# Optimization experiments

Hardware: AMD Instinct MI355X
Metric: run time of the kernel (lower is better)

## Reference

```python
import jax, jax.numpy as jnp
import numpy as np

GAMMA = 0.1
B, C, H, W = 8, 64, 64, 64
CINT = C // 8


def setup_inputs() -> dict:
    key = jax.random.key(0)
    ks = jax.random.split(key, 5)
    x = jax.random.normal(ks[0], (B, C, H, W), dtype=jnp.float32)
    Wq = jax.random.normal(ks[1], (CINT, C), dtype=jnp.float32) * 0.05
    Wk = jax.random.normal(ks[2], (CINT, C), dtype=jnp.float32) * 0.05
    Wv = jax.random.normal(ks[3], (CINT, C), dtype=jnp.float32) * 0.05
    Wout = jax.random.normal(ks[4], (C, CINT), dtype=jnp.float32) * 0.05
    return {"x": x, "Wq": Wq, "Wk": Wk, "Wv": Wv, "Wout": Wout}


def reference(x, Wq, Wk, Wv, Wout):
    b, c, h, w = x.shape
    n = h * w
    cint = Wq.shape[0]
    xf = x.reshape(b, c, n)                               # [B,C,N]
    q = jnp.einsum('ic,bcn->bin', Wq, xf)                 # [B,Cint,N]
    k = jnp.einsum('ic,bcn->bin', Wk, xf)
    v = jnp.einsum('ic,bcn->bin', Wv, xf)
    # scores[b, n, m] = q[b,:,n] . k[b,:,m]; softmax over dim=1 (the n axis)
    scores = jnp.einsum('bin,bim->bnm', q, k) / jnp.sqrt(jnp.asarray(cint, x.dtype))
    att = jax.nn.softmax(scores, axis=1)                  # [B,N,N], softmax over rows
    att_out = jnp.einsum('bin,bnm->bim', v, att)          # [B,Cint,N]
    out = jnp.einsum('ci,bim->bcm', Wout, att_out)        # [B,C,N]
    return x + out.reshape(b, c, h, w) * GAMMA
```

## Files before the change

### kernel.cpp

```cpp
#include <hip/hip_runtime.h>
#include <math.h>

#define BB 8
#define CC 64
#define NN 4096
#define CI 8
#define GAMMA 0.1f
#define SCALE (1.44269504088896f * 0.35355339059327f)
#define NSPLIT 4

typedef float v4f __attribute__((ext_vector_type(4)));
typedef __bf16 bf16x8 __attribute__((ext_vector_type(8)));
typedef __bf16 bf16x4 __attribute__((ext_vector_type(4)));
typedef __bf16 bf16x2 __attribute__((ext_vector_type(2)));

__device__ __forceinline__ float fast_exp2(float x) {
    return __builtin_amdgcn_exp2f(x);
}

__global__ __launch_bounds__(256) void qkv_kernel(
        const float* __restrict__ x,
        const float* __restrict__ Wq, const float* __restrict__ Wk,
        const float* __restrict__ Wv,
        __bf16* __restrict__ qbh, __bf16* __restrict__ kbh,
        __bf16* __restrict__ vbh, float* __restrict__ attab) {
    __shared__ float sw[3 * CI * CC];
    __shared__ unsigned short sq[32 * 8];
    __shared__ unsigned short sk[32 * 8];
    const int t = threadIdx.x;
    const int i  = t >> 5;
    const int nl = t & 31;
    const int b  = blockIdx.y;
    const int n0 = blockIdx.x * 32;

    for (int idx = t; idx < CI * CC; idx += 256) {
        sw[idx]                = Wq[idx];
        sw[CI * CC + idx]      = Wk[idx] * SCALE;
        sw[2 * CI * CC + idx]  = Wv[idx];
    }
    int lin = (blockIdx.y * (NN / 32) + blockIdx.x) * 256 + t;
    for (int idx = lin; idx < BB * 9 * NN; idx += BB * NN * CI) attab[idx] = 0.f;
    __syncthreads();

    const int n = n0 + nl;
    const float* xp = x + ((size_t)b * CC) * NN + n;
    const v4f* wq4 = (const v4f*)(sw + i * CC);
    const v4f* wk4 = (const v4f*)(sw + CI * CC + i * CC);
    const v4f* wv4 = (const v4f*)(sw + 2 * CI * CC + i * CC);
    float qa = 0.f, ka = 0.f, va = 0.f;
#pragma unroll 4
    for (int c4 = 0; c4 < CC / 4; ++c4) {
        v4f wq = wq4[c4], wk = wk4[c4], wv = wv4[c4];
        float x0 = xp[(size_t)(c4 * 4 + 0) * NN];
        float x1 = xp[(size_t)(c4 * 4 + 1) * NN];
        float x2 = xp[(size_t)(c4 * 4 + 2) * NN];
        float x3 = xp[(size_t)(c4 * 4 + 3) * NN];
        qa = fmaf(wq.x, x0, qa); ka = fmaf(wk.x, x0, ka); va = fmaf(wv.x, x0, va);
        qa = fmaf(wq.y, x1, qa); ka = fmaf(wk.y, x1, ka); va = fmaf(wv.y, x1, va);
        qa = fmaf(wq.z, x2, qa); ka = fmaf(wk.z, x2, ka); va = fmaf(wv.z, x2, va);
        qa = fmaf(wq.w, x3, qa); ka = fmaf(wk.w, x3, ka); va = fmaf(wv.w, x3, va);
    }
    __bf16 vb = (__bf16)va;
    vbh[((size_t)b * CI + i) * NN + n] = vb;
    __bf16 qb = (__bf16)qa, kb2 = (__bf16)ka;
    sq[nl * 8 + i] = *(unsigned short*)&qb;
    sk[nl * 8 + i] = *(unsigned short*)&kb2;
    __syncthreads();
    if (t < 32) {
        *(uint4*)(qbh + ((size_t)b * NN + n0 + t) * 8) = *(const uint4*)(sq + t * 8);
        *(uint4*)(kbh + ((size_t)b * NN + n0 + t) * 8) = *(const uint4*)(sk + t * 8);
    }
}

__global__ __launch_bounds__(256) void att_kernel(
        const __bf16* __restrict__ qbh, const __bf16* __restrict__ kbh,
        const __bf16* __restrict__ vbh, float* __restrict__ attab) {
    __shared__ unsigned short eld[4][16 * 36];
    const int t = threadIdx.x;
    const int w    = t >> 6;
    const int l    = t & 63;
    const int quad = l >> 4;
    const int lm   = l & 15;
    const int b  = blockIdx.z;
    const int m0 = blockIdx.x * 64 + w * 16;
    const int nbase = blockIdx.y * (NN / NSPLIT);

    bf16x8 zero8, ones8;
#pragma unroll
    for (int z = 0; z < 8; ++z) { zero8[z] = (__bf16)0.0f; ones8[z] = (__bf16)1.0f; }

    bf16x8 kfrag = zero8;
    if (quad == 0)
        kfrag = *(const bf16x8*)(kbh + ((size_t)b * NN + m0 + lm) * 8);

    const __bf16* vrow = vbh + ((size_t)b * CI + (lm & 7)) * NN;

    v4f accO = {0.f, 0.f, 0.f, 0.f};
    unsigned short* ew = &eld[w][lm * 36];

    for (int ch = 0; ch < (NN / NSPLIT) / 32; ++ch) {
        const int nc = nbase + ch * 32;
        bf16x8 q0 = zero8, q1 = zero8;
        if (quad == 0) {
            q0 = *(const bf16x8*)(qbh + ((size_t)b * NN + nc + lm) * 8);
            q1 = *(const bf16x8*)(qbh + ((size_t)b * NN + nc + 16 + lm) * 8);
        }
        bf16x8 vfrag;
        if (lm < 8)      vfrag = *(const bf16x8*)(vrow + nc + quad * 8);
        else if (lm == 8) vfrag = ones8;
        else              vfrag = zero8;

        v4f s0 = __builtin_amdgcn_mfma_f32_16x16x32_bf16(q0, kfrag, (v4f){0.f,0.f,0.f,0.f}, 0, 0, 0);
        v4f s1 = __builtin_amdgcn_mfma_f32_16x16x32_bf16(q1, kfrag, (v4f){0.f,0.f,0.f,0.f}, 0, 0, 0);

        bf16x2 p;
        p[0] = (__bf16)fast_exp2(s0.x); p[1] = (__bf16)fast_exp2(s0.y);
        *(bf16x2*)(ew + quad * 4 + 0)  = p;
        p[0] = (__bf16)fast_exp2(s0.z); p[1] = (__bf16)fast_exp2(s0.w);
        *(bf16x2*)(ew + quad * 4 + 2)  = p;
        p[0] = (__bf16)fast_exp2(s1.x); p[1] = (__bf16)fast_exp2(s1.y);
        *(bf16x2*)(ew + 16 + quad * 4 + 0) = p;
        p[0] = (__bf16)fast_exp2(s1.z); p[1] = (__bf16)fast_exp2(s1.w);
        *(bf16x2*)(ew + 16 + quad * 4 + 2) = p;

        const unsigned short* er = ew + quad * 8;
        bf16x4 e_lo = *(const bf16x4*)(er);
        bf16x4 e_hi = *(const bf16x4*)(er + 4);
        bf16x8 efrag;
#pragma unroll
        for (int z = 0; z < 4; ++z) { efrag[z] = e_lo[z]; efrag[4 + z] = e_hi[z]; }

        accO = __builtin_amdgcn_mfma_f32_16x16x32_bf16(vfrag, efrag, accO, 0, 0, 0);
    }

    float* ap = attab + (size_t)b * 9 * NN + m0 + lm;
    float av[4] = {accO.x, accO.y, accO.z, accO.w};
#pragma unroll
    for (int r = 0; r < 4; ++r) {
        int i = quad * 4 + r;
        if (i < 9) atomicAdd(ap + (size_t)i * NN, av[r]);
    }
}

__global__ __launch_bounds__(256) void out_kernel(
        const float* __restrict__ x, const float* __restrict__ Wout,
        const float* __restrict__ attab, float* __restrict__ out) {
    const int t = threadIdx.x;
    const int c = blockIdx.y;
    const int b = blockIdx.z;
    const int m = (blockIdx.x * 256 + t) * 4;
    const float* ap = attab + (size_t)b * 9 * NN + m;
    v4f sum = *(const v4f*)(ap + (size_t)8 * NN);
    v4f s = {0.f, 0.f, 0.f, 0.f};
#pragma unroll
    for (int i = 0; i < CI; ++i) {
        float wgt = Wout[c * CI + i];
        v4f a = *(const v4f*)(ap + (size_t)i * NN);
        s.x = fmaf(wgt, a.x, s.x);
        s.y = fmaf(wgt, a.y, s.y);
        s.z = fmaf(wgt, a.z, s.z);
        s.w = fmaf(wgt, a.w, s.w);
    }
    size_t o = ((size_t)b * CC + c) * NN + m;
    v4f xv = *(const v4f*)(x + o);
    v4f r;
    r.x = xv.x + GAMMA * (s.x / sum.x);
    r.y = xv.y + GAMMA * (s.y / sum.y);
    r.z = xv.z + GAMMA * (s.z / sum.z);
    r.w = xv.w + GAMMA * (s.w / sum.w);
    *(v4f*)(out + o) = r;
}

extern "C" void kernel_launch(void* const* d_in, const int* in_sizes, int n_in,
                              void* d_out, int out_size, void* d_ws, size_t ws_size,
                              hipStream_t stream) {
    const float* x    = (const float*)d_in[0];
    const float* Wq   = (const float*)d_in[1];
    const float* Wk   = (const float*)d_in[2];
    const float* Wv   = (const float*)d_in[3];
    const float* Wout = (const float*)d_in[4];
    float* out = (float*)d_out;

    __bf16* qbh = (__bf16*)d_ws;
    __bf16* kbh = qbh + (size_t)BB * NN * 8;
    __bf16* vbh = kbh + (size_t)BB * NN * 8;
    float* attab = (float*)(vbh + (size_t)BB * NN * 8);

    qkv_kernel<<<dim3(NN / 32, BB), 256, 0, stream>>>(x, Wq, Wk, Wv, qbh, kbh, vbh, attab);
    att_kernel<<<dim3(NN / 64, NSPLIT, BB), 256, 0, stream>>>(qbh, kbh, vbh, attab);
    out_kernel<<<dim3(NN / 1024, CC, BB), 256, 0, stream>>>(x, Wout, attab, out);
}
```

Baseline: 114.4 us.

## Fuse three kernels into one persistent cooperative kernel with grid syncs

Merges the QKV projection, attention and output kernels into a single cooperative persistent kernel that uses grid.sync between phases, looping over tiles with a grid sized from occupancy. It also restructures the attention inner loop to process two chunks at a time through double-buffered LDS with wider stores. This removes the launch gaps between kernels, but adds grid-wide barrier cost, a per-call occupancy query on the host, and may lower occupancy because all phases share one register and LDS budget.

```diff
diff --git a/kernel.cpp b/kernel.cpp
--- a/kernel.cpp
+++ b/kernel.cpp
@@ -1,5 +1,8 @@
 #include <hip/hip_runtime.h>
+#include <hip/hip_cooperative_groups.h>
 #include <math.h>
+
+namespace cg = cooperative_groups;
 
 #define BB 8
 #define CC 64
@@ -12,163 +15,168 @@
 typedef float v4f __attribute__((ext_vector_type(4)));
 typedef __bf16 bf16x8 __attribute__((ext_vector_type(8)));
 typedef __bf16 bf16x4 __attribute__((ext_vector_type(4)));
-typedef __bf16 bf16x2 __attribute__((ext_vector_type(2)));
 
 __device__ __forceinline__ float fast_exp2(float x) {
     return __builtin_amdgcn_exp2f(x);
 }
 
-__global__ __launch_bounds__(256) void qkv_kernel(
+__global__ __launch_bounds__(256) void fused_kernel(
         const float* __restrict__ x,
         const float* __restrict__ Wq, const float* __restrict__ Wk,
-        const float* __restrict__ Wv,
+        const float* __restrict__ Wv, const float* __restrict__ Wout,
         __bf16* __restrict__ qbh, __bf16* __restrict__ kbh,
-        __bf16* __restrict__ vbh, float* __restrict__ attab) {
-    __shared__ float sw[3 * CI * CC];
-    __shared__ unsigned short sq[32 * 8];
-    __shared__ unsigned short sk[32 * 8];
+        __bf16* __restrict__ vbh, float* __restrict__ attab,
+        float* __restrict__ out) {
+    __shared__ __align__(16) char smem[10240];
+    cg::grid_group grid = cg::this_grid();
     const int t = threadIdx.x;
-    const int i  = t >> 5;
-    const int nl = t & 31;
-    const int b  = blockIdx.y;
-    const int n0 = blockIdx.x * 32;
-
-    for (int idx = t; idx < CI * CC; idx += 256) {
-        sw[idx]                = Wq[idx];
-        sw[CI * CC + idx]      = Wk[idx] * SCALE;
-        sw[2 * CI * CC + idx]  = Wv[idx];
+    const int nblk = gridDim.x;
+
+    {
+        float* sw = (float*)smem;
+        unsigned short* sq = (unsigned short*)(smem + 6144);
+        unsigned short* sk = sq + 256;
+        for (int idx = blockIdx.x * 256 + t; idx < BB * 9 * NN; idx += nblk * 256)
+            attab[idx] = 0.f;
+        for (int idx = t; idx < CI * CC; idx += 256) {
+            sw[idx]        = Wq[idx];
+            sw[512 + idx]  = Wk[idx] * SCALE;
+            sw[1024 + idx] = Wv[idx];
+        }
+        __syncthreads();
+        const int i  = t >> 5;
+        const int nl = t & 31;
+        for (int tile = blockIdx.x; tile < BB * (NN / 32); tile += nblk) {
+            const int b  = tile >> 7;
+            const int n0 = (tile & 127) * 32;
+            const int n  = n0 + nl;
+            const float* xp = x + ((size_t)b * CC) * NN + n;
+            const v4f* wq4 = (const v4f*)(sw + i * CC);
+            const v4f* wk4 = (const v4f*)(sw + 512 + i * CC);
+            const v4f* wv4 = (const v4f*)(sw + 1024 + i * CC);
+            float qa = 0.f, ka = 0.f, va = 0.f;
+#pragma unroll 4
+            for (int c4 = 0; c4 < CC / 4; ++c4) {
+                v4f wq = wq4[c4], wk = wk4[c4], wv = wv4[c4];
+                float x0 = xp[(size_t)(c4 * 4 + 0) * NN];
+                float x1 = xp[(size_t)(c4 * 4 + 1) * NN];
+                float x2 = xp[(size_t)(c4 * 4 + 2) * NN];
+                float x3 = xp[(size_t)(c4 * 4 + 3) * NN];
+                qa = fmaf(wq.x, x0, qa); ka = fmaf(wk.x, x0, ka); va = fmaf(wv.x, x0, va);
+                qa = fmaf(wq.y, x1, qa); ka = fmaf(wk.y, x1, ka); va = fmaf(wv.y, x1, va);
+                qa = fmaf(wq.z, x2, qa); ka = fmaf(wk.z, x2, ka); va = fmaf(wv.z, x2, va);
+                qa = fmaf(wq.w, x3, qa); ka = fmaf(wk.w, x3, ka); va = fmaf(wv.w, x3, va);
+            }
+            __bf16 vb = (__bf16)va;
+            vbh[((size_t)b * CI + i) * NN + n] = vb;
+            __bf16 qb = (__bf16)qa, kb2 = (__bf16)ka;
+            sq[nl * 8 + i] = *(unsigned short*)&qb;
+            sk[nl * 8 + i] = *(unsigned short*)&kb2;
+            __syncthreads();
+            if (t < 32) {
+                *(uint4*)(qbh + ((size_t)b * NN + n0 + t) * 8) = *(const uint4*)(sq + t * 8);
+                *(uint4*)(kbh + ((size_t)b * NN + n0 + t) * 8) = *(const uint4*)(sk + t * 8);
+            }
+            __syncthreads();
+        }
     }
-    int lin = (blockIdx.y * (NN / 32) + blockIdx.x) * 256 + t;
-    for (int idx = lin; idx < BB * 9 * NN; idx += BB * NN * CI) attab[idx] = 0.f;
-    __syncthreads();
-
-    const int n = n0 + nl;
-    const float* xp = x + ((size_t)b * CC) * NN + n;
-    const v4f* wq4 = (const v4f*)(sw + i * CC);
-    const v4f* wk4 = (const v4f*)(sw + CI * CC + i * CC);
-    const v4f* wv4 = (const v4f*)(sw + 2 * CI * CC + i * CC);
-    float qa = 0.f, ka = 0.f, va = 0.f;
-#pragma unroll 4
-    for (int c4 = 0; c4 < CC / 4; ++c4) {
-        v4f wq = wq4[c4], wk = wk4[c4], wv = wv4[c4];
-        float x0 = xp[(size_t)(c4 * 4 + 0) * NN];
-        float x1 = xp[(size_t)(c4 * 4 + 1) * NN];
-        float x2 = xp[(size_t)(c4 * 4 + 2) * NN];
-        float x3 = xp[(size_t)(c4 * 4 + 3) * NN];
-        qa = fmaf(wq.x, x0, qa); ka = fmaf(wk.x, x0, ka); va = fmaf(wv.x, x0, va);
-        qa = fmaf(wq.y, x1, qa); ka = fmaf(wk.y, x1, ka); va = fmaf(wv.y, x1, va);
-        qa = fmaf(wq.z, x2, qa); ka = fmaf(wk.z, x2, ka); va = fmaf(wv.z, x2, va);
-        qa = fmaf(wq.w, x3, qa); ka = fmaf(wk.w, x3, ka); va = fmaf(wv.w, x3, va);
+    grid.sync();
+
+    {
+        const int w    = t >> 6;
+        const int l    = t & 63;
+        const int quad = l >> 4;
+        const int lm   = l & 15;
+        unsigned short* buf0 = (unsigned short*)smem + w * 1280;
+        unsigned short* buf1 = buf0 + 640;
+
+        bf16x8 zero8, ones8;
+#pragma unroll
+        for (int z = 0; z < 8; ++z) { zero8[z] = (__bf16)0.0f; ones8[z] = (__bf16)1.0f; }
+
+        for (int u = blockIdx.x; u < BB * NSPLIT * (NN / 64); u += nblk) {
+            const int b     = u >> 8;
+            const int nbase = ((u >> 6) & (NSPLIT - 1)) * (NN / NSPLIT);
+            const int m0    = (u & 63) * 64 + w * 16;
+
+            bf16x8 kfrag = zero8;
+            if (quad == 0)
+                kfrag = *(const bf16x8*)(kbh + ((size_t)b * NN + m0 + lm) * 8);
+            const __bf16* vrow = vbh + ((size_t)b * CI + (lm & 7)) * NN;
+            const __bf16* qrow = qbh + (size_t)b * NN * 8;
+
+            v4f accO = {0.f, 0.f, 0.f, 0.f};
+
+            auto stage1 = [&](int nc, unsigned short* buf, bf16x8& vfrag) {
+                bf16x8 q0 = zero8, q1 = zero8;
+                if (quad == 0) {
+                    q0 = *(const bf16x8*)(qrow + (size_t)(nc + lm) * 8);
+                    q1 = *(const bf16x8*)(qrow + (size_t)(nc + 16 + lm) * 8);
+                }
+                if (lm < 8)       vfrag = *(const bf16x8*)(vrow + nc + quad * 8);
+                else if (lm == 8) vfrag = ones8;
+                else              vfrag = zero8;
+                v4f s0 = __builtin_amdgcn_mfma_f32_16x16x32_bf16(q0, kfrag, (v4f){0.f,0.f,0.f,0.f}, 0, 0, 0);
+                v4f s1 = __builtin_amdgcn_mfma_f32_16x16x32_bf16(q1, kfrag, (v4f){0.f,0.f,0.f,0.f}, 0, 0, 0);
+                bf16x4 e0, e1;
+                e0[0] = (__bf16)fast_exp2(s0.x); e0[1] = (__bf16)fast_exp2(s0.y);
+                e0[2] = (__bf16)fast_exp2(s0.z); e0[3] = (__bf16)fast_exp2(s0.w);
+                e1[0] = (__bf16)fast_exp2(s1.x); e1[1] = (__bf16)fast_exp2(s1.y);
+                e1[2] = (__bf16)fast_exp2(s1.z); e1[3] = (__bf16)fast_exp2(s1.w);
+                *(bf16x4*)(buf + lm * 40 + quad * 4)      = e0;
+                *(bf16x4*)(buf + lm * 40 + 16 + quad * 4) = e1;
+            };
+            auto stage2 = [&](unsigned short* buf, bf16x8 vfrag) {
+                bf16x8 efrag = *(const bf16x8*)(buf + lm * 40 + quad * 8);
+                accO = __builtin_amdgcn_mfma_f32_16x16x32_bf16(vfrag, efrag, accO, 0, 0, 0);
+            };
+
+            for (int ch = 0; ch < (NN / NSPLIT) / 32; ch += 2) {
+                bf16x8 vf0, vf1;
+                stage1(nbase + ch * 32, buf0, vf0);
+                stage1(nbase + (ch + 1) * 32, buf1, vf1);
+                stage2(buf0, vf0);
+                stage2(buf1, vf1);
+            }
+
+            float* ap = attab + (size_t)b * 9 * NN + m0 + lm;
+            float av[4] = {accO.x, accO.y, accO.z, accO.w};
+#pragma unroll
+            for (int r = 0; r < 4; ++r) {
+                int i = quad * 4 + r;
+                if (i < 9) atomicAdd(ap + (size_t)i * NN, av[r]);
+            }
+        }
     }
-    __bf16 vb = (__bf16)va;
-    vbh[((size_t)b * CI + i) * NN + n] = vb;
-    __bf16 qb = (__bf16)qa, kb2 = (__bf16)ka;
-    sq[nl * 8 + i] = *(unsigned short*)&qb;
-    sk[nl * 8 + i] = *(unsigned short*)&kb2;
-    __syncthreads();
-    if (t < 32) {
-        *(uint4*)(qbh + ((size_t)b * NN + n0 + t) * 8) = *(const uint4*)(sq + t * 8);
-        *(uint4*)(kbh + ((size_t)b * NN + n0 + t) * 8) = *(const uint4*)(sk + t * 8);
+    grid.sync();
+
+    for (int q = blockIdx.x * 256 + t; q < BB * CC * (NN / 4); q += nblk * 256) {
+        const int m4   = q & (NN / 4 - 1);
+        const int rest = q >> 10;
+        const int c = rest & (CC - 1);
+        const int b = rest >> 6;
+        const int m = m4 * 4;
+        const float* ap = attab + (size_t)b * 9 * NN + m;
+        v4f sum = *(const v4f*)(ap + (size_t)8 * NN);
+        v4f s = {0.f, 0.f, 0.f, 0.f};
+#pragma unroll
+        for (int i = 0; i < CI; ++i) {
+            float wgt = Wout[c * CI + i];
+            v4f a = *(const v4f*)(ap + (size_t)i * NN);
+            s.x = fmaf(wgt, a.x, s.x);
+            s.y = fmaf(wgt, a.y, s.y);
+            s.z = fmaf(wgt, a.z, s.z);
+            s.w = fmaf(wgt, a.w, s.w);
+        }
+        size_t o = ((size_t)b * CC + c) * NN + m;
+        v4f xv = *(const v4f*)(x + o);
+        v4f r;
+        r.x = xv.x + GAMMA * (s.x / sum.x);
+        r.y = xv.y + GAMMA * (s.y / sum.y);
+        r.z = xv.z + GAMMA * (s.z / sum.z);
+        r.w = xv.w + GAMMA * (s.w / sum.w);
+        *(v4f*)(out + o) = r;
     }
-}
-
-__global__ __launch_bounds__(256) void att_kernel(
-        const __bf16* __restrict__ qbh, const __bf16* __restrict__ kbh,
-        const __bf16* __restrict__ vbh, float* __restrict__ attab) {
-    __shared__ unsigned short eld[4][16 * 36];
-    const int t = threadIdx.x;
-    const int w    = t >> 6;
-    const int l    = t & 63;
-    const int quad = l >> 4;
-    const int lm   = l & 15;
-    const int b  = blockIdx.z;
-    const int m0 = blockIdx.x * 64 + w * 16;
-    const int nbase = blockIdx.y * (NN / NSPLIT);
-
-    bf16x8 zero8, ones8;
-#pragma unroll
-    for (int z = 0; z < 8; ++z) { zero8[z] = (__bf16)0.0f; ones8[z] = (__bf16)1.0f; }
-
-    bf16x8 kfrag = zero8;
-    if (quad == 0)
-        kfrag = *(const bf16x8*)(kbh + ((size_t)b * NN + m0 + lm) * 8);
-
-    const __bf16* vrow = vbh + ((size_t)b * CI + (lm & 7)) * NN;
-
-    v4f accO = {0.f, 0.f, 0.f, 0.f};
-    unsigned short* ew = &eld[w][lm * 36];
-
-    for (int ch = 0; ch < (NN / NSPLIT) / 32; ++ch) {
-        const int nc = nbase + ch * 32;
-        bf16x8 q0 = zero8, q1 = zero8;
-        if (quad == 0) {
-            q0 = *(const bf16x8*)(qbh + ((size_t)b * NN + nc + lm) * 8);
-            q1 = *(const bf16x8*)(qbh + ((size_t)b * NN + nc + 16 + lm) * 8);
-        }
-        bf16x8 vfrag;
-        if (lm < 8)      vfrag = *(const bf16x8*)(vrow + nc + quad * 8);
-        else if (lm == 8) vfrag = ones8;
-        else              vfrag = zero8;
-
-        v4f s0 = __builtin_amdgcn_mfma_f32_16x16x32_bf16(q0, kfrag, (v4f){0.f,0.f,0.f,0.f}, 0, 0, 0);
-        v4f s1 = __builtin_amdgcn_mfma_f32_16x16x32_bf16(q1, kfrag, (v4f){0.f,0.f,0.f,0.f}, 0, 0, 0);
-
-        bf16x2 p;
-        p[0] = (__bf16)fast_exp2(s0.x); p[1] = (__bf16)fast_exp2(s0.y);
-        *(bf16x2*)(ew + quad * 4 + 0)  = p;
-        p[0] = (__bf16)fast_exp2(s0.z); p[1] = (__bf16)fast_exp2(s0.w);
-        *(bf16x2*)(ew + quad * 4 + 2)  = p;
-        p[0] = (__bf16)fast_exp2(s1.x); p[1] = (__bf16)fast_exp2(s1.y);
-        *(bf16x2*)(ew + 16 + quad * 4 + 0) = p;
-        p[0] = (__bf16)fast_exp2(s1.z); p[1] = (__bf16)fast_exp2(s1.w);
-        *(bf16x2*)(ew + 16 + quad * 4 + 2) = p;
-
-        const unsigned short* er = ew + quad * 8;
-        bf16x4 e_lo = *(const bf16x4*)(er);
-        bf16x4 e_hi = *(const bf16x4*)(er + 4);
-        bf16x8 efrag;
-#pragma unroll
-        for (int z = 0; z < 4; ++z) { efrag[z] = e_lo[z]; efrag[4 + z] = e_hi[z]; }
-
-        accO = __builtin_amdgcn_mfma_f32_16x16x32_bf16(vfrag, efrag, accO, 0, 0, 0);
-    }
-
-    float* ap = attab + (size_t)b * 9 * NN + m0 + lm;
-    float av[4] = {accO.x, accO.y, accO.z, accO.w};
-#pragma unroll
-    for (int r = 0; r < 4; ++r) {
-        int i = quad * 4 + r;
-        if (i < 9) atomicAdd(ap + (size_t)i * NN, av[r]);
-    }
-}
-
-__global__ __launch_bounds__(256) void out_kernel(
-        const float* __restrict__ x, const float* __restrict__ Wout,
-        const float* __restrict__ attab, float* __restrict__ out) {
-    const int t = threadIdx.x;
-    const int c = blockIdx.y;
-    const int b = blockIdx.z;
-    const int m = (blockIdx.x * 256 + t) * 4;
-    const float* ap = attab + (size_t)b * 9 * NN + m;
-    v4f sum = *(const v4f*)(ap + (size_t)8 * NN);
-    v4f s = {0.f, 0.f, 0.f, 0.f};
-#pragma unroll
-    for (int i = 0; i < CI; ++i) {
-        float wgt = Wout[c * CI + i];
-        v4f a = *(const v4f*)(ap + (size_t)i * NN);
-        s.x = fmaf(wgt, a.x, s.x);
-        s.y = fmaf(wgt, a.y, s.y);
-        s.z = fmaf(wgt, a.z, s.z);
-        s.w = fmaf(wgt, a.w, s.w);
-    }
-    size_t o = ((size_t)b * CC + c) * NN + m;
-    v4f xv = *(const v4f*)(x + o);
-    v4f r;
-    r.x = xv.x + GAMMA * (s.x / sum.x);
-    r.y = xv.y + GAMMA * (s.y / sum.y);
-    r.z = xv.z + GAMMA * (s.z / sum.z);
-    r.w = xv.w + GAMMA * (s.w / sum.w);
-    *(v4f*)(out + o) = r;
 }
 
 extern "C" void kernel_launch(void* const* d_in, const int* in_sizes, int n_in,
@@ -186,7 +194,14 @@
     __bf16* vbh = kbh + (size_t)BB * NN * 8;
     float* attab = (float*)(vbh + (size_t)BB * NN * 8);
 
-    qkv_kernel<<<dim3(NN / 32, BB), 256, 0, stream>>>(x, Wq, Wk, Wv, qbh, kbh, vbh, attab);
-    att_kernel<<<dim3(NN / 64, NSPLIT, BB), 256, 0, stream>>>(qbh, kbh, vbh, attab);
-    out_kernel<<<dim3(NN / 1024, CC, BB), 256, 0, stream>>>(x, Wout, attab, out);
+    int occ = 0;
+    hipOccupancyMaxActiveBlocksPerMultiprocessor(&occ, fused_kernel, 256, 0);
+    if (occ < 1) occ = 1;
+    int gridn = occ * 256;
+    if (gridn > 2048) gridn = 2048;
+
+    void* args[] = {(void*)&x, (void*)&Wq, (void*)&Wk, (void*)&Wv, (void*)&Wout,
+                    (void*)&qbh, (void*)&kbh, (void*)&vbh, (void*)&attab, (void*)&out};
+    hipLaunchCooperativeKernel((const void*)fused_kernel, dim3(gridn), dim3(256),
+                               args, 0, stream);
 }
```

Measured after the change: 239.3 us. 2.09x slower.

## Replace second MFMA with per-lane packed FMA accumulation of exp-weighted V

Applied to the files above, without the earlier changes.

Drops the LDS round trip and the second MFMA that multiplied V by the exp-scores. Each lane now exponentiates its own score elements and accumulates them against fp32 V rows with packed v2 FMAs, then reduces across quads with shuffles before the atomics. V is stored as fp32 in an [n][8] layout so each lane can load contiguous vectors. The V@P product moves from matrix cores to vector ALU work, and V reads per lane grow because fp32 V is loaded for every score element.

```diff
diff --git a/kernel.cpp b/kernel.cpp
--- a/kernel.cpp
+++ b/kernel.cpp
@@ -9,10 +9,9 @@
 #define SCALE (1.44269504088896f * 0.35355339059327f)
 #define NSPLIT 4
 
+typedef float v2f __attribute__((ext_vector_type(2)));
 typedef float v4f __attribute__((ext_vector_type(4)));
 typedef __bf16 bf16x8 __attribute__((ext_vector_type(8)));
-typedef __bf16 bf16x4 __attribute__((ext_vector_type(4)));
-typedef __bf16 bf16x2 __attribute__((ext_vector_type(2)));
 
 __device__ __forceinline__ float fast_exp2(float x) {
     return __builtin_amdgcn_exp2f(x);
@@ -23,10 +22,11 @@
         const float* __restrict__ Wq, const float* __restrict__ Wk,
         const float* __restrict__ Wv,
         __bf16* __restrict__ qbh, __bf16* __restrict__ kbh,
-        __bf16* __restrict__ vbh, float* __restrict__ attab) {
+        float* __restrict__ vf, float* __restrict__ attab) {
     __shared__ float sw[3 * CI * CC];
     __shared__ unsigned short sq[32 * 8];
     __shared__ unsigned short sk[32 * 8];
+    __shared__ float sv[32 * 8];
     const int t = threadIdx.x;
     const int i  = t >> 5;
     const int nl = t & 31;
@@ -60,22 +60,25 @@
         qa = fmaf(wq.z, x2, qa); ka = fmaf(wk.z, x2, ka); va = fmaf(wv.z, x2, va);
         qa = fmaf(wq.w, x3, qa); ka = fmaf(wk.w, x3, ka); va = fmaf(wv.w, x3, va);
     }
-    __bf16 vb = (__bf16)va;
-    vbh[((size_t)b * CI + i) * NN + n] = vb;
     __bf16 qb = (__bf16)qa, kb2 = (__bf16)ka;
     sq[nl * 8 + i] = *(unsigned short*)&qb;
     sk[nl * 8 + i] = *(unsigned short*)&kb2;
+    sv[nl * 8 + i] = va;
     __syncthreads();
     if (t < 32) {
         *(uint4*)(qbh + ((size_t)b * NN + n0 + t) * 8) = *(const uint4*)(sq + t * 8);
         *(uint4*)(kbh + ((size_t)b * NN + n0 + t) * 8) = *(const uint4*)(sk + t * 8);
     }
+    if (t < 64) {
+        int n2 = t >> 1, h = t & 1;
+        *(v4f*)(vf + ((size_t)b * NN + n0 + n2) * 8 + h * 4) =
+            *(const v4f*)(sv + n2 * 8 + h * 4);
+    }
 }
 
 __global__ __launch_bounds__(256) void att_kernel(
         const __bf16* __restrict__ qbh, const __bf16* __restrict__ kbh,
-        const __bf16* __restrict__ vbh, float* __restrict__ attab) {
-    __shared__ unsigned short eld[4][16 * 36];
+        const float* __restrict__ vf, float* __restrict__ attab) {
     const int t = threadIdx.x;
     const int w    = t >> 6;
     const int l    = t & 63;
@@ -85,60 +88,72 @@
     const int m0 = blockIdx.x * 64 + w * 16;
     const int nbase = blockIdx.y * (NN / NSPLIT);
 
-    bf16x8 zero8, ones8;
-#pragma unroll
-    for (int z = 0; z < 8; ++z) { zero8[z] = (__bf16)0.0f; ones8[z] = (__bf16)1.0f; }
+    bf16x8 zero8;
+#pragma unroll
+    for (int z = 0; z < 8; ++z) zero8[z] = (__bf16)0.0f;
 
     bf16x8 kfrag = zero8;
     if (quad == 0)
         kfrag = *(const bf16x8*)(kbh + ((size_t)b * NN + m0 + lm) * 8);
 
-    const __bf16* vrow = vbh + ((size_t)b * CI + (lm & 7)) * NN;
-
-    v4f accO = {0.f, 0.f, 0.f, 0.f};
-    unsigned short* ew = &eld[w][lm * 36];
-
+    const __bf16* qrow = qbh + (size_t)b * NN * 8;
+    const float*  vrow = vf  + (size_t)b * NN * 8;
+
+    v2f acc[4] = {(v2f){0.f,0.f}, (v2f){0.f,0.f}, (v2f){0.f,0.f}, (v2f){0.f,0.f}};
+    float es = 0.f;
+
+#pragma unroll 2
     for (int ch = 0; ch < (NN / NSPLIT) / 32; ++ch) {
         const int nc = nbase + ch * 32;
         bf16x8 q0 = zero8, q1 = zero8;
         if (quad == 0) {
-            q0 = *(const bf16x8*)(qbh + ((size_t)b * NN + nc + lm) * 8);
-            q1 = *(const bf16x8*)(qbh + ((size_t)b * NN + nc + 16 + lm) * 8);
+            q0 = *(const bf16x8*)(qrow + (size_t)(nc + lm) * 8);
+            q1 = *(const bf16x8*)(qrow + (size_t)(nc + 16 + lm) * 8);
         }
-        bf16x8 vfrag;
-        if (lm < 8)      vfrag = *(const bf16x8*)(vrow + nc + quad * 8);
-        else if (lm == 8) vfrag = ones8;
-        else              vfrag = zero8;
-
         v4f s0 = __builtin_amdgcn_mfma_f32_16x16x32_bf16(q0, kfrag, (v4f){0.f,0.f,0.f,0.f}, 0, 0, 0);
         v4f s1 = __builtin_amdgcn_mfma_f32_16x16x32_bf16(q1, kfrag, (v4f){0.f,0.f,0.f,0.f}, 0, 0, 0);
 
-        bf16x2 p;
-        p[0] = (__bf16)fast_exp2(s0.x); p[1] = (__bf16)fast_exp2(s0.y);
-        *(bf16x2*)(ew + quad * 4 + 0)  = p;
-        p[0] = (__bf16)fast_exp2(s0.z); p[1] = (__bf16)fast_exp2(s0.w);
-        *(bf16x2*)(ew + quad * 4 + 2)  = p;
-        p[0] = (__bf16)fast_exp2(s1.x); p[1] = (__bf16)fast_exp2(s1.y);
-        *(bf16x2*)(ew + 16 + quad * 4 + 0) = p;
-        p[0] = (__bf16)fast_exp2(s1.z); p[1] = (__bf16)fast_exp2(s1.w);
-        *(bf16x2*)(ew + 16 + quad * 4 + 2) = p;
-
-        const unsigned short* er = ew + quad * 8;
-        bf16x4 e_lo = *(const bf16x4*)(er);
-        bf16x4 e_hi = *(const bf16x4*)(er + 4);
-        bf16x8 efrag;
-#pragma unroll
-        for (int z = 0; z < 4; ++z) { efrag[z] = e_lo[z]; efrag[4 + z] = e_hi[z]; }
-
-        accO = __builtin_amdgcn_mfma_f32_16x16x32_bf16(vfrag, efrag, accO, 0, 0, 0);
-    }
-
-    float* ap = attab + (size_t)b * 9 * NN + m0 + lm;
-    float av[4] = {accO.x, accO.y, accO.z, accO.w};
-#pragma unroll
-    for (int r = 0; r < 4; ++r) {
-        int i = quad * 4 + r;
-        if (i < 9) atomicAdd(ap + (size_t)i * NN, av[r]);
+        const float* vp0 = vrow + (size_t)(nc + quad * 4) * 8;
+        const float* vp1 = vrow + (size_t)(nc + 16 + quad * 4) * 8;
+        float sv0[4] = {s0.x, s0.y, s0.z, s0.w};
+        float sv1[4] = {s1.x, s1.y, s1.z, s1.w};
+#pragma unroll
+        for (int r = 0; r < 4; ++r) {
+            float e = fast_exp2(sv0[r]);
+            es += e;
+            v4f vlo = *(const v4f*)(vp0 + r * 8);
+            v4f vhi = *(const v4f*)(vp0 + r * 8 + 4);
+            v2f e2 = {e, e};
+            acc[0] = __builtin_elementwise_fma(e2, (v2f){vlo.x, vlo.y}, acc[0]);
+            acc[1] = __builtin_elementwise_fma(e2, (v2f){vlo.z, vlo.w}, acc[1]);
+            acc[2] = __builtin_elementwise_fma(e2, (v2f){vhi.x, vhi.y}, acc[2]);
+            acc[3] = __builtin_elementwise_fma(e2, (v2f){vhi.z, vhi.w}, acc[3]);
+        }
+#pragma unroll
+        for (int r = 0; r < 4; ++r) {
+            float e = fast_exp2(sv1[r]);
+            es += e;
+            v4f vlo = *(const v4f*)(vp1 + r * 8);
+            v4f vhi = *(const v4f*)(vp1 + r * 8 + 4);
+            v2f e2 = {e, e};
+            acc[0] = __builtin_elementwise_fma(e2, (v2f){vlo.x, vlo.y}, acc[0]);
+            acc[1] = __builtin_elementwise_fma(e2, (v2f){vlo.z, vlo.w}, acc[1]);
+            acc[2] = __builtin_elementwise_fma(e2, (v2f){vhi.x, vhi.y}, acc[2]);
+            acc[3] = __builtin_elementwise_fma(e2, (v2f){vhi.z, vhi.w}, acc[3]);
+        }
+    }
+
+    float vals[9] = {acc[0].x, acc[0].y, acc[1].x, acc[1].y,
+                     acc[2].x, acc[2].y, acc[3].x, acc[3].y, es};
+#pragma unroll
+    for (int i = 0; i < 9; ++i) {
+        vals[i] += __shfl_xor(vals[i], 16);
+        vals[i] += __shfl_xor(vals[i], 32);
+    }
+    if (quad == 0) {
+        float* ap = attab + (size_t)b * 9 * NN + m0 + lm;
+#pragma unroll
+        for (int i = 0; i < 9; ++i) atomicAdd(ap + (size_t)i * NN, vals[i]);
     }
 }
 
@@ -183,10 +198,10 @@
 
     __bf16* qbh = (__bf16*)d_ws;
     __bf16* kbh = qbh + (size_t)BB * NN * 8;
-    __bf16* vbh = kbh + (size_t)BB * NN * 8;
-    float* attab = (float*)(vbh + (size_t)BB * NN * 8);
-
-    qkv_kernel<<<dim3(NN / 32, BB), 256, 0, stream>>>(x, Wq, Wk, Wv, qbh, kbh, vbh, attab);
-    att_kernel<<<dim3(NN / 64, NSPLIT, BB), 256, 0, stream>>>(qbh, kbh, vbh, attab);
+    float*  vf  = (float*)(kbh + (size_t)BB * NN * 8);
+    float* attab = vf + (size_t)BB * NN * 8;
+
+    qkv_kernel<<<dim3(NN / 32, BB), 256, 0, stream>>>(x, Wq, Wk, Wv, qbh, kbh, vf, attab);
+    att_kernel<<<dim3(NN / 64, NSPLIT, BB), 256, 0, stream>>>(qbh, kbh, vf, attab);
     out_kernel<<<dim3(NN / 1024, CC, BB), 256, 0, stream>>>(x, Wout, attab, out);
 }
```

Result: slower. 211.2 us (+84.6%).

## Use 32x32x16 MFMA for score tiles with 32 columns per wave

Applied to the files above, without the earlier changes.

The attention kernel now computes each score tile with a single 32x32x16 bf16 MFMA instead of two 16x16x32 MFMAs. This lets each wave cover 32 key columns and use every lane for the exp work, where before only one quad loaded Q. Each P·V step now issues two 16x16 MFMAs that share one V fragment, and the split over n is doubled to keep the grid size the same. The goal is to cut wasted MFMA work on zero-padded operands and amortise V loads, at the cost of a larger LDS tile and twice as many atomic adds per block.

```diff
diff --git a/kernel.cpp b/kernel.cpp
--- a/kernel.cpp
+++ b/kernel.cpp
@@ -7,12 +7,12 @@
 #define CI 8
 #define GAMMA 0.1f
 #define SCALE (1.44269504088896f * 0.35355339059327f)
-#define NSPLIT 4
+#define NSPLIT 8
 
-typedef float v4f __attribute__((ext_vector_type(4)));
+typedef float v4f  __attribute__((ext_vector_type(4)));
+typedef float v16f __attribute__((ext_vector_type(16)));
 typedef __bf16 bf16x8 __attribute__((ext_vector_type(8)));
 typedef __bf16 bf16x4 __attribute__((ext_vector_type(4)));
-typedef __bf16 bf16x2 __attribute__((ext_vector_type(2)));
 
 __device__ __forceinline__ float fast_exp2(float x) {
     return __builtin_amdgcn_exp2f(x);
@@ -75,70 +75,77 @@
 __global__ __launch_bounds__(256) void att_kernel(
         const __bf16* __restrict__ qbh, const __bf16* __restrict__ kbh,
         const __bf16* __restrict__ vbh, float* __restrict__ attab) {
-    __shared__ unsigned short eld[4][16 * 36];
+    __shared__ unsigned short eld[4][32 * 36];
     const int t = threadIdx.x;
     const int w    = t >> 6;
     const int l    = t & 63;
+    const int ln   = l & 31;
+    const int hi   = l >> 5;
     const int quad = l >> 4;
     const int lm   = l & 15;
     const int b  = blockIdx.z;
-    const int m0 = blockIdx.x * 64 + w * 16;
+    const int m0 = blockIdx.x * 128 + w * 32;
     const int nbase = blockIdx.y * (NN / NSPLIT);
+    const int NCH = (NN / NSPLIT) / 32;
 
     bf16x8 zero8, ones8;
 #pragma unroll
     for (int z = 0; z < 8; ++z) { zero8[z] = (__bf16)0.0f; ones8[z] = (__bf16)1.0f; }
 
-    bf16x8 kfrag = zero8;
-    if (quad == 0)
-        kfrag = *(const bf16x8*)(kbh + ((size_t)b * NN + m0 + lm) * 8);
+    bf16x8 kfragB = hi ? zero8
+                       : *(const bf16x8*)(kbh + ((size_t)b * NN + m0 + ln) * 8);
 
+    const __bf16* qrow = qbh + (size_t)b * NN * 8;
     const __bf16* vrow = vbh + ((size_t)b * CI + (lm & 7)) * NN;
+    const bool v_v = (lm < 8);
+    const bool v_1 = (lm == 8);
 
-    v4f accO = {0.f, 0.f, 0.f, 0.f};
-    unsigned short* ew = &eld[w][lm * 36];
+    unsigned short* tile = eld[w];
+    unsigned short* wr   = tile + ln * 36 + hi * 4;
+    const unsigned short* rd0 = tile + lm * 36 + quad * 8;
+    const unsigned short* rd1 = tile + (16 + lm) * 36 + quad * 8;
 
-    for (int ch = 0; ch < (NN / NSPLIT) / 32; ++ch) {
+    v4f acc0 = {0.f, 0.f, 0.f, 0.f};
+    v4f acc1 = {0.f, 0.f, 0.f, 0.f};
+
+    for (int ch = 0; ch < NCH; ++ch) {
         const int nc = nbase + ch * 32;
-        bf16x8 q0 = zero8, q1 = zero8;
-        if (quad == 0) {
-            q0 = *(const bf16x8*)(qbh + ((size_t)b * NN + nc + lm) * 8);
-            q1 = *(const bf16x8*)(qbh + ((size_t)b * NN + nc + 16 + lm) * 8);
+        bf16x8 qfrag = hi ? zero8
+                          : *(const bf16x8*)(qrow + (size_t)(nc + ln) * 8);
+        bf16x8 vfrag = v_v ? *(const bf16x8*)(vrow + nc + quad * 8)
+                           : (v_1 ? ones8 : zero8);
+
+        v16f S = __builtin_amdgcn_mfma_f32_32x32x16_bf16(
+            qfrag, kfragB,
+            (v16f){0.f,0.f,0.f,0.f,0.f,0.f,0.f,0.f,0.f,0.f,0.f,0.f,0.f,0.f,0.f,0.f},
+            0, 0, 0);
+
+#pragma unroll
+        for (int g = 0; g < 4; ++g) {
+            bf16x4 e;
+            e[0] = (__bf16)fast_exp2(S[4 * g + 0]);
+            e[1] = (__bf16)fast_exp2(S[4 * g + 1]);
+            e[2] = (__bf16)fast_exp2(S[4 * g + 2]);
+            e[3] = (__bf16)fast_exp2(S[4 * g + 3]);
+            *(bf16x4*)(wr + g * 8) = e;
         }
-        bf16x8 vfrag;
-        if (lm < 8)      vfrag = *(const bf16x8*)(vrow + nc + quad * 8);
-        else if (lm == 8) vfrag = ones8;
-        else              vfrag = zero8;
 
-        v4f s0 = __builtin_amdgcn_mfma_f32_16x16x32_bf16(q0, kfrag, (v4f){0.f,0.f,0.f,0.f}, 0, 0, 0);
-        v4f s1 = __builtin_amdgcn_mfma_f32_16x16x32_bf16(q1, kfrag, (v4f){0.f,0.f,0.f,0.f}, 0, 0, 0);
-
-        bf16x2 p;
-        p[0] = (__bf16)fast_exp2(s0.x); p[1] = (__bf16)fast_exp2(s0.y);
-        *(bf16x2*)(ew + quad * 4 + 0)  = p;
-        p[0] = (__bf16)fast_exp2(s0.z); p[1] = (__bf16)fast_exp2(s0.w);
-        *(bf16x2*)(ew + quad * 4 + 2)  = p;
-        p[0] = (__bf16)fast_exp2(s1.x); p[1] = (__bf16)fast_exp2(s1.y);
-        *(bf16x2*)(ew + 16 + quad * 4 + 0) = p;
-        p[0] = (__bf16)fast_exp2(s1.z); p[1] = (__bf16)fast_exp2(s1.w);
-        *(bf16x2*)(ew + 16 + quad * 4 + 2) = p;
-
-        const unsigned short* er = ew + quad * 8;
-        bf16x4 e_lo = *(const bf16x4*)(er);
-        bf16x4 e_hi = *(const bf16x4*)(er + 4);
-        bf16x8 efrag;
-#pragma unroll
-        for (int z = 0; z < 4; ++z) { efrag[z] = e_lo[z]; efrag[4 + z] = e_hi[z]; }
-
-        accO = __builtin_amdgcn_mfma_f32_16x16x32_bf16(vfrag, efrag, accO, 0, 0, 0);
+        bf16x8 ef0 = *(const bf16x8*)(rd0);
+        bf16x8 ef1 = *(const bf16x8*)(rd1);
+        acc0 = __builtin_amdgcn_mfma_f32_16x16x32_bf16(vfrag, ef0, acc0, 0, 0, 0);
+        acc1 = __builtin_amdgcn_mfma_f32_16x16x32_bf16(vfrag, ef1, acc1, 0, 0, 0);
     }
 
-    float* ap = attab + (size_t)b * 9 * NN + m0 + lm;
-    float av[4] = {accO.x, accO.y, accO.z, accO.w};
+    float* ap = attab + (size_t)b * 9 * NN + m0;
+    float a0[4] = {acc0.x, acc0.y, acc0.z, acc0.w};
+    float a1[4] = {acc1.x, acc1.y, acc1.z, acc1.w};
 #pragma unroll
     for (int r = 0; r < 4; ++r) {
         int i = quad * 4 + r;
-        if (i < 9) atomicAdd(ap + (size_t)i * NN, av[r]);
+        if (i < 9) {
+            atomicAdd(ap + (size_t)i * NN + lm, a0[r]);
+            atomicAdd(ap + (size_t)i * NN + 16 + lm, a1[r]);
+        }
     }
 }
 
@@ -187,6 +194,6 @@
     float* attab = (float*)(vbh + (size_t)BB * NN * 8);
 
     qkv_kernel<<<dim3(NN / 32, BB), 256, 0, stream>>>(x, Wq, Wk, Wv, qbh, kbh, vbh, attab);
-    att_kernel<<<dim3(NN / 64, NSPLIT, BB), 256, 0, stream>>>(qbh, kbh, vbh, attab);
+    att_kernel<<<dim3(NN / 128, NSPLIT, BB), 256, 0, stream>>>(qbh, kbh, vbh, attab);
     out_kernel<<<dim3(NN / 1024, CC, BB), 256, 0, stream>>>(x, Wout, attab, out);
 }
```

After: 113.5 us. No clear change (-0.7%).
